# Kernel tuning notes

Measured on AMD Instinct MI355X. Metric: run time of the kernel, lower is better.

## Reference

```python
import jax, jax.numpy as jnp
import numpy as np


def _cdist(a, b):
    # a: [B, N, D], b: [B, M, D] -> [B, N, M] Euclidean distances
    sq = (jnp.sum(a * a, -1)[:, :, None]
          + jnp.sum(b * b, -1)[:, None, :]
          - 2.0 * jnp.einsum('bnd,bmd->bnm', a, b))
    return jnp.sqrt(jnp.maximum(sq, 1e-12))


def setup_inputs() -> dict:
    key = jax.random.key(0)
    k1, k2, k3, k4 = jax.random.split(key, 4)
    B, N, NC, S = 2, 32768, 1024, 32
    centers = jax.random.normal(k1, (B, NC, 3), dtype=jnp.float32)
    radius = jax.random.uniform(k2, (B, NC, 1), dtype=jnp.float32)
    xyz = jax.random.normal(k3, (B, N, 3), dtype=jnp.float32)
    sphere_points = jax.random.normal(k4, (B, NC * S, 3), dtype=jnp.float32)
    return {"centers": centers, "radius": radius, "xyz": xyz,
            "sphere_points": sphere_points}


def reference(centers, radius, xyz, sphere_points):
    B, NC, _ = centers.shape
    # point -> center distances  [B, N, NC]
    dmat = _cdist(xyz, centers)
    cd_p_to_c = jnp.min(dmat, axis=-1)            # [B, N]
    idx_p_to_c = jnp.argmin(dmat, axis=-1)        # [B, N]
    # gather radius of nearest center for each point
    radius_from_p = jnp.take_along_axis(radius[..., 0], idx_p_to_c, axis=1)  # [B, N]
    # is_surface=False branch: clamp positive diffs to 0, then mean(|.|)
    diff = jnp.minimum(radius_from_p - cd_p_to_c, 0.0)
    radius_difference_p_to_c = jnp.mean(jnp.abs(diff), axis=1)               # [B]
    # sphere-point -> sample distances  [B, N, NC*S]
    dmat_sp = _cdist(xyz, sphere_points)
    cd_sp_to_p = jnp.min(dmat_sp, axis=1)          # [B, NC*S]
    max_cd_sp_to_p = jnp.max(cd_sp_to_p.reshape(B, NC, -1), axis=-1)         # [B, NC]
    radius_difference_c_to_p = jnp.mean(jnp.abs(max_cd_sp_to_p), axis=1)     # [B]
    res = radius_difference_c_to_p + radius_difference_p_to_c
    return jnp.mean(res)  # reduction='mean'
```

## Files before the change

### kernel.cpp

```cpp
#include <hip/hip_runtime.h>

#define B   2
#define N   32768
#define NC  1024
#define S   32
#define NSP (NC * S)

#define CHUNK 2048
#define NCH   (N / CHUNK)
#define BLKT  512
#define COLS_BLK 512
#define GRIDX (NSP / COLS_BLK)

typedef __attribute__((ext_vector_type(8)))  short short8v;
typedef __attribute__((ext_vector_type(16))) float f32x16;
typedef const __attribute__((address_space(1))) void gvoid_t;
typedef __attribute__((address_space(3))) void svoid_t;

static __device__ __forceinline__ unsigned short f2b(float x) {
    unsigned u = __float_as_uint(x);
    return (unsigned short)((u + 0x7FFFu + ((u >> 16) & 1u)) >> 16);
}
static __device__ __forceinline__ float b2f(unsigned short u) {
    return __uint_as_float(((unsigned)u) << 16);
}
static __device__ __forceinline__ float min3f(float a, float b, float c) {
    return fminf(fminf(a, b), c);
}


__global__ __launch_bounds__(256) void k_prep(const float* __restrict__ xyz,
                                              unsigned short* __restrict__ Afrag,
                                              unsigned long long* __restrict__ best,
                                              unsigned* __restrict__ minsq,
                                              unsigned* __restrict__ accw) {
    int i = blockIdx.x * 256 + threadIdx.x;
    if (i < 2) accw[i] = 0u;
    best[i]  = ~0ull;
    minsq[i] = 0x7F800000u;

    const float* q = xyz + (size_t)i * 3;
    float qx = q[0], qy = q[1], qz = q[2];
    float h = 0.5f * (qx * qx + qy * qy + qz * qz);
    unsigned short xh = f2b(-qx), yh = f2b(-qy), zh = f2b(-qz);
    unsigned short xl = f2b(-qx - b2f(xh));
    unsigned short yl = f2b(-qy - b2f(yh));
    unsigned short zl = f2b(-qz - b2f(zh));
    unsigned short hh = f2b(h), hl = f2b(h - b2f(hh));

    int b = i >> 15, j = i & (N - 1);
    int tile = j >> 5, r = j & 31;
    unsigned short* base = Afrag + ((size_t)b * N + (size_t)tile * 32) * 16;
    uint4 s0, s1;
    s0.x = (unsigned)xh | ((unsigned)yh << 16);
    s0.y = (unsigned)zh | ((unsigned)xl << 16);
    s0.z = (unsigned)yl | ((unsigned)zl << 16);
    s0.w = (unsigned)xh | ((unsigned)yh << 16);
    s1.x = (unsigned)zh | ((unsigned)hh << 16);
    s1.y = (unsigned)hl;
    s1.z = 0u; s1.w = 0u;
    *(uint4*)(base + (size_t)r * 8)        = s0;
    *(uint4*)(base + (size_t)(r + 32) * 8) = s1;
}

__global__ __launch_bounds__(256) void k_p2c(const float* __restrict__ centers,
                                             const float* __restrict__ xyz,
                                             unsigned long long* __restrict__ best) {
    __shared__ float4 c4[256];
    const int b = blockIdx.z, qb = blockIdx.y, tid = threadIdx.x;

    const float* cb = centers + ((size_t)b * NC + qb * 256) * 3;
    for (int g = tid; g < 64; g += 256) {
        float4 f0 = ((const float4*)cb)[g * 3 + 0];
        float4 f1 = ((const float4*)cb)[g * 3 + 1];
        float4 f2 = ((const float4*)cb)[g * 3 + 2];
        float x0 = f0.x, y0 = f0.y, z0 = f0.z;
        float x1 = f0.w, y1 = f1.x, z1 = f1.y;
        float x2 = f1.z, y2 = f1.w, z2 = f2.x;
        float x3 = f2.y, y3 = f2.z, z3 = f2.w;
        c4[g * 4 + 0] = make_float4(x0, y0, z0, 0.5f * (x0 * x0 + y0 * y0 + z0 * z0));
        c4[g * 4 + 1] = make_float4(x1, y1, z1, 0.5f * (x1 * x1 + y1 * y1 + z1 * z1));
        c4[g * 4 + 2] = make_float4(x2, y2, z2, 0.5f * (x2 * x2 + y2 * y2 + z2 * z2));
        c4[g * 4 + 3] = make_float4(x3, y3, z3, 0.5f * (x3 * x3 + y3 * y3 + z3 * z3));
    }
    __syncthreads();

    const int pi = blockIdx.x * 256 + tid;
    const float* p = xyz + ((size_t)b * N + pi) * 3;
    const float px = p[0], py = p[1], pz = p[2];

    float tmin = 1e30f;
    int   imin = 0;
    #pragma unroll 4
    for (int c = 0; c < 256; ++c) {
        float4 q = c4[c];
        float  t = q.w - px * q.x - py * q.y - pz * q.z;
        if (t < tmin) { tmin = t; imin = c; }
    }
    unsigned bits = __float_as_uint(tmin);
    unsigned ord  = (bits & 0x80000000u) ? ~bits : (bits | 0x80000000u);
    unsigned long long key =
        ((unsigned long long)ord << 32) | (unsigned)(qb * 256 + imin);
    atomicMin(best + (size_t)b * N + pi, key);
}

__global__ __launch_bounds__(BLKT) void k_sp2p(const float* __restrict__ sp,
                                               const unsigned short* __restrict__ Afrag,
                                               unsigned* __restrict__ minsq) {
    __shared__ unsigned short lds[CHUNK * 16];
    const int b = blockIdx.z, chunk = blockIdx.y;
    const int tid = threadIdx.x, wid = tid >> 6, lane = tid & 63;

    const char* src = (const char*)(Afrag +
                        ((size_t)b * N + (size_t)chunk * CHUNK) * 16);
    #pragma unroll
    for (int it = 0; it < 8; ++it) {
        int off = it * 8192 + wid * 1024;
        __builtin_amdgcn_global_load_lds((gvoid_t*)(src + off + lane * 16),
                                         (svoid_t*)((char*)lds + off), 16, 0, 0);
    }

    const int colbase = blockIdx.x * COLS_BLK + wid * 64 + (lane & 31);
    float pp[2]; short8v bf[2];
    #pragma unroll
    for (int f = 0; f < 2; ++f) {
        const float* p = sp + ((size_t)b * NSP + colbase + f * 32) * 3;
        float px = p[0], py = p[1], pz = p[2];
        pp[f] = px * px + py * py + pz * pz;
        unsigned short xh = f2b(px), yh = f2b(py), zh = f2b(pz);
        unsigned short xl = f2b(px - b2f(xh));
        unsigned short yl = f2b(py - b2f(yh));
        unsigned short zl = f2b(pz - b2f(zh));
        short8v v;
        if (lane < 32) {
            v[0] = (short)xh; v[1] = (short)yh; v[2] = (short)zh;
            v[3] = (short)xh; v[4] = (short)yh; v[5] = (short)zh;
            v[6] = (short)xl; v[7] = (short)yl;
        } else {
            v[0] = (short)zl; v[1] = (short)0x3F80; v[2] = (short)0x3F80;
            v[3] = 0; v[4] = 0; v[5] = 0; v[6] = 0; v[7] = 0;
        }
        bf[f] = v;
    }
    f32x16 zero;
    #pragma unroll
    for (int i = 0; i < 16; ++i) zero[i] = 0.0f;

    __syncthreads();

    float run0 = 1e30f, run1 = 1e30f;
    const unsigned short* ap = lds + lane * 8;
    #pragma unroll 4
    for (int t = 0; t < CHUNK / 32; ++t) {
        short8v a = *(const short8v*)(ap + (size_t)t * 512);
        f32x16 a0 = __builtin_amdgcn_mfma_f32_32x32x16_bf16(a, bf[0], zero, 0, 0, 0);
        f32x16 a1 = __builtin_amdgcn_mfma_f32_32x32x16_bf16(a, bf[1], zero, 0, 0, 0);
        {
            float m0 = min3f(a0[0], a0[1], a0[2]);
            float m1 = min3f(a0[3], a0[4], a0[5]);
            float m2 = min3f(a0[6], a0[7], a0[8]);
            float m3 = min3f(a0[9], a0[10], a0[11]);
            float m4 = min3f(a0[12], a0[13], a0[14]);
            float n0 = min3f(m0, m1, a0[15]);
            float n1 = min3f(m2, m3, m4);
            run0 = min3f(run0, n0, n1);
        }
        {
            float m0 = min3f(a1[0], a1[1], a1[2]);
            float m1 = min3f(a1[3], a1[4], a1[5]);
            float m2 = min3f(a1[6], a1[7], a1[8]);
            float m3 = min3f(a1[9], a1[10], a1[11]);
            float m4 = min3f(a1[12], a1[13], a1[14]);
            float n0 = min3f(m0, m1, a1[15]);
            float n1 = min3f(m2, m3, m4);
            run1 = min3f(run1, n0, n1);
        }
    }

    run0 = fminf(run0, __shfl_xor(run0, 32, 64));
    run1 = fminf(run1, __shfl_xor(run1, 32, 64));
    if (lane < 32) {
        float sq0 = fmaxf(2.0f * run0 + pp[0], 0.0f);
        float sq1 = fmaxf(2.0f * run1 + pp[1], 0.0f);
        unsigned* mb = minsq + (size_t)b * NSP + colbase;
        atomicMin(mb,      __float_as_uint(sq0));
        atomicMin(mb + 32, __float_as_uint(sq1));
    }
}

__global__ __launch_bounds__(256) void k_fin(const unsigned long long* __restrict__ best,
                                             const unsigned* __restrict__ minsq,
                                             const float* __restrict__ xyz,
                                             const float* __restrict__ radius,
                                             float* __restrict__ acc,
                                             unsigned* __restrict__ counter,
                                             float* __restrict__ out) {
    const int tid = threadIdx.x;
    const int i = blockIdx.x * 256 + tid;
    const int b = i >> 15;

    unsigned long long k = best[i];
    int idx = (int)(k & 0xFFFFFFFFu);
    unsigned ord  = (unsigned)(k >> 32);
    unsigned bits = (ord & 0x80000000u) ? (ord ^ 0x80000000u) : ~ord;
    float tmin = __uint_as_float(bits);
    const float* p = xyz + (size_t)i * 3;
    float pp = p[0] * p[0] + p[1] * p[1] + p[2] * p[2];
    float cdp = sqrtf(fmaxf(2.0f * tmin + pp, 1e-12f));
    float val = fmaxf(cdp - radius[(size_t)b * NC + idx], 0.0f);

    float cd = sqrtf(fmaxf(__uint_as_float(minsq[i]), 1e-12f));
    #pragma unroll
    for (int o = 16; o > 0; o >>= 1) cd = fmaxf(cd, __shfl_xor(cd, o, 64));

    float contrib = val * (1.0f / N) +
                    (((tid & 31) == 0) ? cd * (1.0f / NC) : 0.0f);
    #pragma unroll
    for (int o = 32; o > 0; o >>= 1) contrib += __shfl_down(contrib, o);
    __shared__ float wsum[4];
    if ((tid & 63) == 0) wsum[tid >> 6] = contrib;
    __syncthreads();
    if (tid == 0) atomicAdd(&acc[0], wsum[0] + wsum[1] + wsum[2] + wsum[3]);

    __shared__ int lastf;
    if (tid == 0) {
        __threadfence();
        unsigned old = atomicAdd(counter, 1u);
        lastf = (old == (unsigned)(gridDim.x - 1));
    }
    __syncthreads();
    if (lastf && tid == 0)
        out[0] = atomicAdd(&acc[0], 0.0f) * (1.0f / B);
}

extern "C" void kernel_launch(void* const* d_in, const int* in_sizes, int n_in,
                              void* d_out, int out_size, void* d_ws, size_t ws_size,
                              hipStream_t stream) {
    const float* centers = (const float*)d_in[0];
    const float* radius  = (const float*)d_in[1];
    const float* xyz     = (const float*)d_in[2];
    const float* sp      = (const float*)d_in[3];
    float* out = (float*)d_out;

    unsigned short*     Afrag = (unsigned short*)d_ws;
    unsigned long long* best  = (unsigned long long*)((char*)d_ws + (size_t)B * N * 32);
    unsigned* minsq  = (unsigned*)((char*)best + (size_t)B * N * 8);
    float*    acc    = (float*)((char*)minsq + (size_t)B * NSP * 4);
    unsigned* counter = (unsigned*)acc + 1;

    hipLaunchKernelGGL(k_prep, dim3(B * N / 256), dim3(256), 0, stream,
                       xyz, Afrag, best, minsq, (unsigned*)acc);
    hipLaunchKernelGGL(k_p2c, dim3(N / 256, NC / 256, B), dim3(256), 0, stream,
                       centers, xyz, best);
    hipLaunchKernelGGL(k_sp2p, dim3(GRIDX, NCH, B), dim3(BLKT), 0, stream,
                       sp, Afrag, minsq);
    hipLaunchKernelGGL(k_fin, dim3(B * N / 256), dim3(256), 0, stream,
                       best, minsq, xyz, radius, acc, counter, out);
}
```

Before: 145.2 us.

## Register-block more points per thread in p2c and more MFMA column fragments in sp2p

After: 158.5 us. +9.1%, slower.

```diff
diff --git a/kernel.cpp b/kernel.cpp
--- a/kernel.cpp
+++ b/kernel.cpp
@@ -9,8 +9,12 @@
 #define CHUNK 2048
 #define NCH   (N / CHUNK)
 #define BLKT  512
-#define COLS_BLK 512
+#define FR    4
+#define COLS_BLK (8 * FR * 32)
 #define GRIDX (NSP / COLS_BLK)
+
+#define PJ  8
+#define CSL 256
 
 typedef __attribute__((ext_vector_type(8)))  short short8v;
 typedef __attribute__((ext_vector_type(16))) float f32x16;
@@ -66,11 +70,11 @@
 __global__ __launch_bounds__(256) void k_p2c(const float* __restrict__ centers,
                                              const float* __restrict__ xyz,
                                              unsigned long long* __restrict__ best) {
-    __shared__ float4 c4[256];
+    __shared__ float4 c4[CSL];
     const int b = blockIdx.z, qb = blockIdx.y, tid = threadIdx.x;
 
-    const float* cb = centers + ((size_t)b * NC + qb * 256) * 3;
-    for (int g = tid; g < 64; g += 256) {
+    const float* cb = centers + ((size_t)b * NC + qb * CSL) * 3;
+    for (int g = tid; g < CSL / 4; g += 256) {
         float4 f0 = ((const float4*)cb)[g * 3 + 0];
         float4 f1 = ((const float4*)cb)[g * 3 + 1];
         float4 f2 = ((const float4*)cb)[g * 3 + 2];
@@ -85,23 +89,36 @@
     }
     __syncthreads();
 
-    const int pi = blockIdx.x * 256 + tid;
-    const float* p = xyz + ((size_t)b * N + pi) * 3;
-    const float px = p[0], py = p[1], pz = p[2];
-
-    float tmin = 1e30f;
-    int   imin = 0;
-    #pragma unroll 4
-    for (int c = 0; c < 256; ++c) {
+    const int pbase = blockIdx.x * (256 * PJ) + tid;
+    float px[PJ], py[PJ], pz[PJ], tmin[PJ];
+    int imin[PJ];
+    #pragma unroll
+    for (int k = 0; k < PJ; ++k) {
+        const float* p = xyz + ((size_t)b * N + pbase + k * 256) * 3;
+        px[k] = p[0]; py[k] = p[1]; pz[k] = p[2];
+        tmin[k] = 1e30f; imin[k] = 0;
+    }
+
+    #pragma unroll 2
+    for (int c = 0; c < CSL; ++c) {
         float4 q = c4[c];
-        float  t = q.w - px * q.x - py * q.y - pz * q.z;
-        if (t < tmin) { tmin = t; imin = c; }
-    }
-    unsigned bits = __float_as_uint(tmin);
-    unsigned ord  = (bits & 0x80000000u) ? ~bits : (bits | 0x80000000u);
-    unsigned long long key =
-        ((unsigned long long)ord << 32) | (unsigned)(qb * 256 + imin);
-    atomicMin(best + (size_t)b * N + pi, key);
+        #pragma unroll
+        for (int k = 0; k < PJ; ++k) {
+            float t = q.w - px[k] * q.x - py[k] * q.y - pz[k] * q.z;
+            bool lt = t < tmin[k];
+            tmin[k] = lt ? t : tmin[k];
+            imin[k] = lt ? c : imin[k];
+        }
+    }
+
+    #pragma unroll
+    for (int k = 0; k < PJ; ++k) {
+        unsigned bits = __float_as_uint(tmin[k]);
+        unsigned ord  = (bits & 0x80000000u) ? ~bits : (bits | 0x80000000u);
+        unsigned long long key =
+            ((unsigned long long)ord << 32) | (unsigned)(qb * CSL + imin[k]);
+        atomicMin(best + (size_t)b * N + pbase + k * 256, key);
+    }
 }
 
 __global__ __launch_bounds__(BLKT) void k_sp2p(const float* __restrict__ sp,
@@ -120,17 +137,17 @@
                                          (svoid_t*)((char*)lds + off), 16, 0, 0);
     }
 
-    const int colbase = blockIdx.x * COLS_BLK + wid * 64 + (lane & 31);
-    float pp[2]; short8v bf[2];
-    #pragma unroll
-    for (int f = 0; f < 2; ++f) {
+    const int colbase = blockIdx.x * COLS_BLK + wid * (FR * 32) + (lane & 31);
+    float pp[FR]; short8v bf[FR];
+    #pragma unroll
+    for (int f = 0; f < FR; ++f) {
         const float* p = sp + ((size_t)b * NSP + colbase + f * 32) * 3;
-        float px = p[0], py = p[1], pz = p[2];
-        pp[f] = px * px + py * py + pz * pz;
-        unsigned short xh = f2b(px), yh = f2b(py), zh = f2b(pz);
-        unsigned short xl = f2b(px - b2f(xh));
-        unsigned short yl = f2b(py - b2f(yh));
-        unsigned short zl = f2b(pz - b2f(zh));
+        float qx = p[0], qy = p[1], qz = p[2];
+        pp[f] = qx * qx + qy * qy + qz * qz;
+        unsigned short xh = f2b(qx), yh = f2b(qy), zh = f2b(qz);
+        unsigned short xl = f2b(qx - b2f(xh));
+        unsigned short yl = f2b(qy - b2f(yh));
+        unsigned short zl = f2b(qz - b2f(zh));
         short8v v;
         if (lane < 32) {
             v[0] = (short)xh; v[1] = (short)yh; v[2] = (short)zh;
@@ -146,45 +163,40 @@
     #pragma unroll
     for (int i = 0; i < 16; ++i) zero[i] = 0.0f;
 
-    __syncthreads();
-
-    float run0 = 1e30f, run1 = 1e30f;
+    float run[FR];
+    #pragma unroll
+    for (int f = 0; f < FR; ++f) run[f] = 1e30f;
+
+    __syncthreads();
+
     const unsigned short* ap = lds + lane * 8;
-    #pragma unroll 4
+    #pragma unroll 1
     for (int t = 0; t < CHUNK / 32; ++t) {
         short8v a = *(const short8v*)(ap + (size_t)t * 512);
-        f32x16 a0 = __builtin_amdgcn_mfma_f32_32x32x16_bf16(a, bf[0], zero, 0, 0, 0);
-        f32x16 a1 = __builtin_amdgcn_mfma_f32_32x32x16_bf16(a, bf[1], zero, 0, 0, 0);
-        {
-            float m0 = min3f(a0[0], a0[1], a0[2]);
-            float m1 = min3f(a0[3], a0[4], a0[5]);
-            float m2 = min3f(a0[6], a0[7], a0[8]);
-            float m3 = min3f(a0[9], a0[10], a0[11]);
-            float m4 = min3f(a0[12], a0[13], a0[14]);
-            float n0 = min3f(m0, m1, a0[15]);
-            float n1 = min3f(m2, m3, m4);
-            run0 = min3f(run0, n0, n1);
-        }
-        {
-            float m0 = min3f(a1[0], a1[1], a1[2]);
-            float m1 = min3f(a1[3], a1[4], a1[5]);
-            float m2 = min3f(a1[6], a1[7], a1[8]);
-            float m3 = min3f(a1[9], a1[10], a1[11]);
-            float m4 = min3f(a1[12], a1[13], a1[14]);
-            float n0 = min3f(m0, m1, a1[15]);
-            float n1 = min3f(m2, m3, m4);
-            run1 = min3f(run1, n0, n1);
-        }
-    }
-
-    run0 = fminf(run0, __shfl_xor(run0, 32, 64));
-    run1 = fminf(run1, __shfl_xor(run1, 32, 64));
+        #pragma unroll
+        for (int f = 0; f < FR; ++f) {
+            f32x16 d = __builtin_amdgcn_mfma_f32_32x32x16_bf16(a, bf[f], zero, 0, 0, 0);
+            float r0 = min3f(d[0],  d[1],  d[2]);
+            float r1 = min3f(d[3],  d[4],  d[5]);
+            float r2 = min3f(d[6],  d[7],  d[8]);
+            float r3 = min3f(d[9],  d[10], d[11]);
+            float r4 = min3f(d[12], d[13], d[14]);
+            float r5 = min3f(r0, r1, d[15]);
+            float r6 = min3f(r2, r3, r4);
+            run[f] = min3f(run[f], r5, r6);
+        }
+    }
+
+    #pragma unroll
+    for (int f = 0; f < FR; ++f)
+        run[f] = fminf(run[f], __shfl_xor(run[f], 32, 64));
     if (lane < 32) {
-        float sq0 = fmaxf(2.0f * run0 + pp[0], 0.0f);
-        float sq1 = fmaxf(2.0f * run1 + pp[1], 0.0f);
         unsigned* mb = minsq + (size_t)b * NSP + colbase;
-        atomicMin(mb,      __float_as_uint(sq0));
-        atomicMin(mb + 32, __float_as_uint(sq1));
+        #pragma unroll
+        for (int f = 0; f < FR; ++f) {
+            float sq = fmaxf(2.0f * run[f] + pp[f], 0.0f);
+            atomicMin(mb + f * 32, __float_as_uint(sq));
+        }
     }
 }
 
@@ -250,7 +262,7 @@
 
     hipLaunchKernelGGL(k_prep, dim3(B * N / 256), dim3(256), 0, stream,
                        xyz, Afrag, best, minsq, (unsigned*)acc);
-    hipLaunchKernelGGL(k_p2c, dim3(N / 256, NC / 256, B), dim3(256), 0, stream,
+    hipLaunchKernelGGL(k_p2c, dim3(N / (256 * PJ), NC / CSL, B), dim3(256), 0, stream,
                        centers, xyz, best);
     hipLaunchKernelGGL(k_sp2p, dim3(GRIDX, NCH, B), dim3(BLKT), 0, stream,
                        sp, Afrag, minsq);
```
